# Performance work log

Measured on AMD Instinct MI355X. Metric: run time of the kernel, lower is better.

Reference implementation:

```python
import jax, jax.numpy as jnp
import numpy as np

BN_EPS = 1e-5


def _conv_bn_elu(x, w, b, bn_scale, bn_bias, bn_mean, bn_var):
    # 1x1 conv == channel-mixing matmul: x [B,C,H,W], w [O,C]
    y = jnp.einsum('bchw,oc->bohw', x, w) + b[None, :, None, None]
    inv = bn_scale * jax.lax.rsqrt(bn_var + BN_EPS)
    y = y * inv[None, :, None, None] + (bn_bias - bn_mean * inv)[None, :, None, None]
    return jax.nn.elu(y)


def setup_inputs() -> dict:
    key = jax.random.key(0)
    ks = jax.random.split(key, 24)
    B, C, H, W = 4, 128, 64, 64
    d = {}
    d['x_q'] = jax.random.normal(ks[0], (B, C, H, W), jnp.float32)
    d['x_k'] = jax.random.normal(ks[1], (B, C, H, W), jnp.float32)
    d['x_v'] = jax.random.normal(ks[2], (B, C, H, W), jnp.float32)
    scale = 1.0 / np.sqrt(C)
    i = 3
    for p in ('q', 'k', 'v'):
        d[f'{p}_w'] = jax.random.normal(ks[i], (C, C), jnp.float32) * scale; i += 1
        d[f'{p}_b'] = jax.random.normal(ks[i], (C,), jnp.float32) * 0.01; i += 1
        d[f'{p}_bn_scale'] = jnp.ones((C,), jnp.float32) + 0.1 * jax.random.normal(ks[i], (C,), jnp.float32); i += 1
        d[f'{p}_bn_bias'] = 0.1 * jax.random.normal(ks[i], (C,), jnp.float32); i += 1
        d[f'{p}_bn_mean'] = 0.1 * jax.random.normal(ks[i], (C,), jnp.float32); i += 1
        d[f'{p}_bn_var'] = jax.random.uniform(ks[i], (C,), jnp.float32, 0.5, 1.5); i += 1
    # torch inits gamma/beta to zero; use small nonzero values so output is informative
    d['gamma'] = jnp.array([0.5], jnp.float32)
    d['beta'] = jnp.array([0.5], jnp.float32)
    return d


def reference(x_q, x_k, x_v,
              q_w, q_b, q_bn_scale, q_bn_bias, q_bn_mean, q_bn_var,
              k_w, k_b, k_bn_scale, k_bn_bias, k_bn_mean, k_bn_var,
              v_w, v_b, v_bn_scale, v_bn_bias, v_bn_mean, v_bn_var,
              gamma, beta):
    B, C, Hv, Wv = x_v.shape
    q = _conv_bn_elu(x_q, q_w, q_b, q_bn_scale, q_bn_bias, q_bn_mean, q_bn_var).reshape(B, C, -1)  # [B,C,HWq]
    k = _conv_bn_elu(x_k, k_w, k_b, k_bn_scale, k_bn_bias, k_bn_mean, k_bn_var).reshape(B, C, -1)  # [B,C,HWk]
    v = _conv_bn_elu(x_v, v_w, v_b, v_bn_scale, v_bn_bias, v_bn_mean, v_bn_var).reshape(B, C, -1)  # [B,C,HWv]
    energy = jnp.einsum('bcq,bck->bqk', q, k)                 # [B,HWq,HWk] (no scaling, as in source)
    attention = jax.nn.softmax(energy, axis=-1)
    out = jnp.einsum('bck,bqk->bcq', v, attention)            # [B,C,HWq]
    out = out.reshape(B, C, Hv, Wv)
    return gamma * out + beta * x_v
```

## Files before the change

kernel.cpp:

```cpp
#include <hip/hip_runtime.h>

#define CC 128
#define SS 4096
#define L2E 1.44269504f

typedef _Float16 f16;
typedef f16 f16x8 __attribute__((ext_vector_type(8)));
typedef __fp16 h16x2 __attribute__((ext_vector_type(2)));
typedef float f32x4 __attribute__((ext_vector_type(4)));

struct PArg { const float *x, *w, *b, *sc, *bb, *bm, *bv; f16* out; };

__global__ __launch_bounds__(256) void projk(PArg A0, PArg A1, PArg A2) {
    const int p = blockIdx.y;
    PArg A = (p == 0) ? A0 : ((p == 1) ? A1 : A2);
    const int bx = blockIdx.x;
    const int b  = bx >> 6;
    const int s0 = (bx & 63) * 64;
    const int tid = threadIdx.x;
    const int w = tid >> 6, lane = tid & 63;
    const int n = lane & 15, g = lane >> 4;

    __shared__ f16 Xl[64][136];
    __shared__ f16 Wl[128][136];
    f16* Yl = &Wl[0][0];

#pragma unroll
    for (int i = 0; i < 8; ++i) {
        int vi = tid + i * 256;
        int c = vi >> 4, sq = (vi & 15) * 4;
        float4 v = *(const float4*)(A.x + ((size_t)b * CC + c) * SS + s0 + sq);
        Xl[sq + 0][c] = (f16)v.x; Xl[sq + 1][c] = (f16)v.y;
        Xl[sq + 2][c] = (f16)v.z; Xl[sq + 3][c] = (f16)v.w;
    }
#pragma unroll
    for (int i = 0; i < 8; ++i) {
        int vi = tid + i * 256;
        int o = vi >> 4, cq = (vi & 15) * 8;
        float iv = A.sc[o] * rsqrtf(A.bv[o] + 1e-5f);
        const float* wp = A.w + o * CC + cq;
        float4 a = *(const float4*)wp;
        float4 b4 = *(const float4*)(wp + 4);
        union { f16 h[8]; uint4 u; } pk;
        pk.h[0] = (f16)(a.x * iv);  pk.h[1] = (f16)(a.y * iv);
        pk.h[2] = (f16)(a.z * iv);  pk.h[3] = (f16)(a.w * iv);
        pk.h[4] = (f16)(b4.x * iv); pk.h[5] = (f16)(b4.y * iv);
        pk.h[6] = (f16)(b4.z * iv); pk.h[7] = (f16)(b4.w * iv);
        *(uint4*)&Wl[o][cq] = pk.u;
    }
    __syncthreads();

    if (p < 2) {
        const float qsc = (p == 0) ? L2E : 1.0f;
        f32x4 acc[2][4];
#pragma unroll
        for (int mt = 0; mt < 2; ++mt)
#pragma unroll
            for (int nt = 0; nt < 4; ++nt) acc[mt][nt] = (f32x4){0.f, 0.f, 0.f, 0.f};
#pragma unroll
        for (int ks = 0; ks < 4; ++ks) {
            f16x8 af[2], bf[4];
#pragma unroll
            for (int mt = 0; mt < 2; ++mt) af[mt] = *(const f16x8*)&Wl[w * 32 + mt * 16 + n][ks * 32 + g * 8];
#pragma unroll
            for (int nt = 0; nt < 4; ++nt) bf[nt] = *(const f16x8*)&Xl[nt * 16 + n][ks * 32 + g * 8];
#pragma unroll
            for (int mt = 0; mt < 2; ++mt)
#pragma unroll
                for (int nt = 0; nt < 4; ++nt)
                    acc[mt][nt] = __builtin_amdgcn_mfma_f32_16x16x32_f16(af[mt], bf[nt], acc[mt][nt], 0, 0, 0);
        }
        __syncthreads();
#pragma unroll
        for (int mt = 0; mt < 2; ++mt) {
            float ebr[4];
#pragma unroll
            for (int r = 0; r < 4; ++r) {
                int o = w * 32 + mt * 16 + g * 4 + r;
                float iv = A.sc[o] * rsqrtf(A.bv[o] + 1e-5f);
                ebr[r] = (A.b[o] - A.bm[o]) * iv + A.bb[o];
            }
#pragma unroll
            for (int nt = 0; nt < 4; ++nt) {
                union { f16 h[4]; uint2 u; } pk;
#pragma unroll
                for (int r = 0; r < 4; ++r) {
                    float y = acc[mt][nt][r] + ebr[r];
                    y = (y > 0.f) ? y : (__expf(y) - 1.f);
                    pk.h[r] = (f16)(y * qsc);
                }
                *(uint2*)&Yl[(nt * 16 + n) * 136 + w * 32 + mt * 16 + g * 4] = pk.u;
            }
        }
        __syncthreads();
#pragma unroll
        for (int i = 0; i < 4; ++i) {
            int vi = tid + i * 256;
            int s = vi >> 4, cl = (vi & 15) * 8;
            *(uint4*)&A.out[((size_t)b * SS + s0 + s) * CC + cl] = *(const uint4*)&Yl[s * 136 + cl];
        }
    } else {
        f32x4 acc[8];
#pragma unroll
        for (int nt = 0; nt < 8; ++nt) acc[nt] = (f32x4){0.f, 0.f, 0.f, 0.f};
#pragma unroll
        for (int ks = 0; ks < 4; ++ks) {
            f16x8 af = *(const f16x8*)&Xl[w * 16 + n][ks * 32 + g * 8];
#pragma unroll
            for (int nt = 0; nt < 8; ++nt) {
                f16x8 bf = *(const f16x8*)&Wl[nt * 16 + n][ks * 32 + g * 8];
                acc[nt] = __builtin_amdgcn_mfma_f32_16x16x32_f16(af, bf, acc[nt], 0, 0, 0);
            }
        }
        __syncthreads();
#pragma unroll
        for (int nt = 0; nt < 8; ++nt) {
            int o = nt * 16 + n;
            float iv = A.sc[o] * rsqrtf(A.bv[o] + 1e-5f);
            float ebc = (A.b[o] - A.bm[o]) * iv + A.bb[o];
            union { f16 h[4]; uint2 u; } pk;
#pragma unroll
            for (int r = 0; r < 4; ++r) {
                float y = acc[nt][r] + ebc;
                y = (y > 0.f) ? y : (__expf(y) - 1.f);
                pk.h[r] = (f16)y;
            }
            *(uint2*)&Yl[(nt * 16 + n) * 136 + w * 16 + g * 4] = pk.u;
        }
        __syncthreads();
#pragma unroll
        for (int i = 0; i < 4; ++i) {
            int vi = tid + i * 256;
            int o = vi >> 3, sl = (vi & 7) * 8;
            *(uint4*)&A.out[((size_t)b * CC + o) * SS + s0 + sl] = *(const uint4*)&Yl[o * 136 + sl];
        }
    }
}

__global__ __launch_bounds__(256, 3) void attnk(
    const f16* __restrict__ Qt, const f16* __restrict__ Kt, const f16* __restrict__ Vt,
    f16* __restrict__ Op, float* __restrict__ Ml)
{
    const int tid = threadIdx.x;
    const int bx = blockIdx.x;
    const int kh = bx & 7;
    const int b  = (bx >> 3) & 3;
    const int qt = bx >> 5;
    const int q0 = qt * 128;
    const int kbeg = kh * 512;

    __shared__ __align__(16) char arena[48128];
    const int w = tid >> 6, lane = tid & 63;
    const int n = lane & 15, g = lane >> 4;
    f16 (*Pw)[40] = (f16(*)[40])(arena + 37888 + w * 2560);

    f16x8 qf[2][4];
    {
        const f16* Qb = Qt + ((size_t)b * SS + q0 + w * 32) * CC;
#pragma unroll
        for (int qt2 = 0; qt2 < 2; ++qt2)
#pragma unroll
            for (int ks = 0; ks < 4; ++ks)
                qf[qt2][ks] = *(const f16x8*)&Qb[(qt2 * 16 + n) * CC + ks * 32 + g * 8];
    }

    f32x4 oacc[8][2];
#pragma unroll
    for (int mtc = 0; mtc < 8; ++mtc)
#pragma unroll
        for (int qt2 = 0; qt2 < 2; ++qt2) oacc[mtc][qt2] = (f32x4){0.f, 0.f, 0.f, 0.f};
    float mreg[2] = {-1e30f, -1e30f}, lsum[2] = {0.f, 0.f};

    const int rk0 = tid >> 4,        ck0 = (tid & 15) * 8;
    const int rk1 = (tid + 256) >> 4, ck1 = ((tid + 256) & 15) * 8;
    const int rv0 = tid >> 2,        cv0 = (tid & 3) * 8;
    const int rv1 = (tid + 256) >> 2, cv1 = ((tid + 256) & 3) * 8;

    {
        f16 (*Kl)[136] = (f16(*)[136])(arena);
        f16 (*Vl)[40]  = (f16(*)[40])(arena + 17408);
        *(uint4*)&Kl[rk0][ck0] = *(const uint4*)&Kt[((size_t)b * SS + kbeg + rk0) * CC + ck0];
        *(uint4*)&Kl[rk1][ck1] = *(const uint4*)&Kt[((size_t)b * SS + kbeg + rk1) * CC + ck1];
        *(uint4*)&Vl[rv0][cv0] = *(const uint4*)&Vt[((size_t)b * CC + rv0) * SS + kbeg + cv0];
        *(uint4*)&Vl[rv1][cv1] = *(const uint4*)&Vt[((size_t)b * CC + rv1) * SS + kbeg + cv1];
    }

    for (int kt = 0; kt < 16; ++kt) {
        const int cur = kt & 1;
        f16 (*Kl)[136] = (f16(*)[136])(arena + cur * 8704);
        f16 (*Vl)[40]  = (f16(*)[40])(arena + 17408 + cur * 10240);
        f16 (*Kn)[136] = (f16(*)[136])(arena + (1 - cur) * 8704);
        f16 (*Vn)[40]  = (f16(*)[40])(arena + 17408 + (1 - cur) * 10240);

        __syncthreads();

        uint4 nk0, nk1, nv0, nv1;
        if (kt < 15) {
            const int k1 = kbeg + (kt + 1) * 32;
            nk0 = *(const uint4*)&Kt[((size_t)b * SS + k1 + rk0) * CC + ck0];
            nk1 = *(const uint4*)&Kt[((size_t)b * SS + k1 + rk1) * CC + ck1];
            nv0 = *(const uint4*)&Vt[((size_t)b * CC + rv0) * SS + k1 + cv0];
            nv1 = *(const uint4*)&Vt[((size_t)b * CC + rv1) * SS + k1 + cv1];
        }

        f32x4 sacc[2][2];
#pragma unroll
        for (int kt2 = 0; kt2 < 2; ++kt2)
#pragma unroll
            for (int qt2 = 0; qt2 < 2; ++qt2) sacc[kt2][qt2] = (f32x4){0.f, 0.f, 0.f, 0.f};
#pragma unroll
        for (int ks = 0; ks < 4; ++ks) {
            f16x8 kf[2];
#pragma unroll
            for (int kt2 = 0; kt2 < 2; ++kt2) kf[kt2] = *(const f16x8*)&Kl[kt2 * 16 + n][ks * 32 + g * 8];
#pragma unroll
            for (int kt2 = 0; kt2 < 2; ++kt2)
#pragma unroll
                for (int qt2 = 0; qt2 < 2; ++qt2)
                    sacc[kt2][qt2] = __builtin_amdgcn_mfma_f32_16x16x32_f16(kf[kt2], qf[qt2][ks], sacc[kt2][qt2], 0, 0, 0);
        }

        if (kt < 15) {
            *(uint4*)&Kn[rk0][ck0] = nk0;
            *(uint4*)&Kn[rk1][ck1] = nk1;
            *(uint4*)&Vn[rv0][cv0] = nv0;
            *(uint4*)&Vn[rv1][cv1] = nv1;
        }

        float al[2];
#pragma unroll
        for (int qt2 = 0; qt2 < 2; ++qt2) {
            float v = sacc[0][qt2][0];
#pragma unroll
            for (int kt2 = 0; kt2 < 2; ++kt2)
#pragma unroll
                for (int r = 0; r < 4; ++r) v = fmaxf(v, sacc[kt2][qt2][r]);
            v = fmaxf(v, __shfl_xor(v, 16));
            v = fmaxf(v, __shfl_xor(v, 32));
            float mn = fmaxf(mreg[qt2], v);
            al[qt2] = exp2f(mreg[qt2] - mn);
            mreg[qt2] = mn;
            float rs = 0.f;
#pragma unroll
            for (int kt2 = 0; kt2 < 2; ++kt2) {
                float p0 = exp2f(sacc[kt2][qt2][0] - mn);
                float p1 = exp2f(sacc[kt2][qt2][1] - mn);
                float p2 = exp2f(sacc[kt2][qt2][2] - mn);
                float p3 = exp2f(sacc[kt2][qt2][3] - mn);
                rs += (p0 + p1) + (p2 + p3);
                union { h16x2 h[2]; uint2 u; } pk;
                pk.h[0] = __builtin_amdgcn_cvt_pkrtz(p0, p1);
                pk.h[1] = __builtin_amdgcn_cvt_pkrtz(p2, p3);
                *(uint2*)&Pw[qt2 * 16 + n][kt2 * 16 + g * 4] = pk.u;
            }
            lsum[qt2] = lsum[qt2] * al[qt2] + rs;
        }
#pragma unroll
        for (int mtc = 0; mtc < 8; ++mtc)
#pragma unroll
            for (int qt2 = 0; qt2 < 2; ++qt2)
#pragma unroll
                for (int r = 0; r < 4; ++r) oacc[mtc][qt2][r] *= al[qt2];

        {
            f16x8 pf[2];
#pragma unroll
            for (int qt2 = 0; qt2 < 2; ++qt2) pf[qt2] = *(const f16x8*)&Pw[qt2 * 16 + n][g * 8];
#pragma unroll
            for (int mtc = 0; mtc < 8; ++mtc) {
                f16x8 vf = *(const f16x8*)&Vl[mtc * 16 + n][g * 8];
#pragma unroll
                for (int qt2 = 0; qt2 < 2; ++qt2)
                    oacc[mtc][qt2] = __builtin_amdgcn_mfma_f32_16x16x32_f16(vf, pf[qt2], oacc[mtc][qt2], 0, 0, 0);
            }
        }
    }

    float lreg[2];
#pragma unroll
    for (int qt2 = 0; qt2 < 2; ++qt2) {
        float s = lsum[qt2];
        s += __shfl_xor(s, 16);
        s += __shfl_xor(s, 32);
        lreg[qt2] = s;
    }

    const int pidx = (b * 32 + qt) * 8 + kh;
    if (g == 0) {
        float* MlW = Ml + (size_t)pidx * 256;
#pragma unroll
        for (int qt2 = 0; qt2 < 2; ++qt2) {
            int q = w * 32 + qt2 * 16 + n;
            MlW[q]       = mreg[qt2];
            MlW[128 + q] = lreg[qt2];
        }
    }

    __syncthreads();
    f16 (*S2)[136] = (f16(*)[136])arena;
#pragma unroll
    for (int mtc = 0; mtc < 8; ++mtc)
#pragma unroll
        for (int qt2 = 0; qt2 < 2; ++qt2)
#pragma unroll
            for (int r = 0; r < 4; ++r)
                S2[mtc * 16 + g * 4 + r][w * 32 + qt2 * 16 + n] = (f16)oacc[mtc][qt2][r];
    __syncthreads();
    f16* OpW = Op + (size_t)pidx * 16384;
#pragma unroll
    for (int i = 0; i < 8; ++i) {
        int vi = tid + i * 256;
        int c = vi >> 4, qq = (vi & 15) * 8;
        *(uint4*)&OpW[c * 128 + qq] = *(const uint4*)&S2[c][qq];
    }
}

__global__ __launch_bounds__(256) void mrgk(
    const f16* __restrict__ Op, const float* __restrict__ Ml,
    const float* __restrict__ xv, const float* __restrict__ gp, const float* __restrict__ bp,
    float* __restrict__ out)
{
    const int bx = blockIdx.x;
    const int cg = bx & 3, bqt = bx >> 2;
    const int b = bqt >> 5, qt = bqt & 31;
    const int tid = threadIdx.x;

    __shared__ float winv[8][128];

    if (tid < 128) {
        const int q = tid;
        const float* ml = Ml + (size_t)bqt * 8 * 256;
        float m = -1e30f;
#pragma unroll
        for (int k2 = 0; k2 < 8; ++k2) m = fmaxf(m, ml[k2 * 256 + q]);
        float wt[8], tot = 0.f;
#pragma unroll
        for (int k2 = 0; k2 < 8; ++k2) {
            wt[k2] = exp2f(ml[k2 * 256 + q] - m);
            tot += wt[k2] * ml[k2 * 256 + 128 + q];
        }
        float inv = 1.f / tot;
#pragma unroll
        for (int k2 = 0; k2 < 8; ++k2) winv[k2][q] = wt[k2] * inv;
    }
    __syncthreads();

    const float gm = gp[0], bb = bp[0];
    const int cl = tid >> 4, qg = tid & 15;
    const f16* O = Op + (size_t)bqt * 8 * 16384;

#pragma unroll
    for (int cp = 0; cp < 2; ++cp) {
        const int c = cg * 32 + cp * 16 + cl;
        float acc[8];
#pragma unroll
        for (int j = 0; j < 8; ++j) acc[j] = 0.f;
#pragma unroll
        for (int k2 = 0; k2 < 8; ++k2) {
            union { uint4 u; f16 h[8]; } ov;
            ov.u = *(const uint4*)&O[k2 * 16384 + c * 128 + qg * 8];
            float4 wa = *(const float4*)&winv[k2][qg * 8];
            float4 wb = *(const float4*)&winv[k2][qg * 8 + 4];
            acc[0] += wa.x * (float)ov.h[0];
            acc[1] += wa.y * (float)ov.h[1];
            acc[2] += wa.z * (float)ov.h[2];
            acc[3] += wa.w * (float)ov.h[3];
            acc[4] += wb.x * (float)ov.h[4];
            acc[5] += wb.y * (float)ov.h[5];
            acc[6] += wb.z * (float)ov.h[6];
            acc[7] += wb.w * (float)ov.h[7];
        }
        size_t idx = ((size_t)(b * CC + c)) * SS + qt * 128 + qg * 8;
        float4 xa = *(const float4*)&xv[idx];
        float4 xb = *(const float4*)&xv[idx + 4];
        float4 oa = { gm * acc[0] + bb * xa.x, gm * acc[1] + bb * xa.y,
                      gm * acc[2] + bb * xa.z, gm * acc[3] + bb * xa.w };
        float4 ob = { gm * acc[4] + bb * xb.x, gm * acc[5] + bb * xb.y,
                      gm * acc[6] + bb * xb.z, gm * acc[7] + bb * xb.w };
        *(float4*)&out[idx]     = oa;
        *(float4*)&out[idx + 4] = ob;
    }
}

extern "C" void kernel_launch(void* const* d_in, const int* in_sizes, int n_in,
                              void* d_out, int out_size, void* d_ws, size_t ws_size,
                              hipStream_t stream) {
    (void)in_sizes; (void)n_in; (void)out_size; (void)ws_size;

    const size_t TEN = (size_t)4 * SS * CC;
    f16* Qt = (f16*)d_ws;
    f16* Kt = Qt + TEN;
    f16* Vt = Kt + TEN;
    f16* Op = Vt + TEN;
    float* Ml = (float*)(Op + (size_t)1024 * 16384);

    PArg aq = { (const float*)d_in[0], (const float*)d_in[3],  (const float*)d_in[4],
                (const float*)d_in[5], (const float*)d_in[6],  (const float*)d_in[7],
                (const float*)d_in[8],  Qt };
    PArg ak = { (const float*)d_in[1], (const float*)d_in[9],  (const float*)d_in[10],
                (const float*)d_in[11], (const float*)d_in[12], (const float*)d_in[13],
                (const float*)d_in[14], Kt };
    PArg av = { (const float*)d_in[2], (const float*)d_in[15], (const float*)d_in[16],
                (const float*)d_in[17], (const float*)d_in[18], (const float*)d_in[19],
                (const float*)d_in[20], Vt };

    hipLaunchKernelGGL(projk, dim3(256, 3), dim3(256), 0, stream, aq, ak, av);
    hipLaunchKernelGGL(attnk, dim3(1024), dim3(256), 0, stream, Qt, Kt, Vt, Op, Ml);
    hipLaunchKernelGGL(mrgk, dim3(512), dim3(256), 0, stream,
                       Op, Ml, (const float*)d_in[2], (const float*)d_in[21],
                       (const float*)d_in[22], (float*)d_out);
}
```

Baseline: 182.4 us.

## Use direct global-to-LDS loads with XOR-swizzled K/V/P tiles in attention

Replaces the register-staged K/V prefetch (global load into registers, later store to LDS) with global_load_lds 16-byte direct-to-LDS loads. Padded LDS rows are replaced by XOR-swizzled unpadded layouts for K, V and the P scratch tile, which shrinks the LDS arena. The aim is to cut register pressure and VGPR-to-LDS store instructions and to avoid bank conflicts, possibly allowing more overlap. It relies on the direct-LDS load write pattern (per-wave contiguous placement) matching the swizzle, and the synchronization must still order those async writes before their reads.

```diff
diff --git a/kernel.cpp b/kernel.cpp
--- a/kernel.cpp
+++ b/kernel.cpp
@@ -8,6 +8,12 @@
 typedef f16 f16x8 __attribute__((ext_vector_type(8)));
 typedef __fp16 h16x2 __attribute__((ext_vector_type(2)));
 typedef float f32x4 __attribute__((ext_vector_type(4)));
+
+__device__ __forceinline__ void gld16(const void* g, void* l) {
+    __builtin_amdgcn_global_load_lds(
+        (const __attribute__((address_space(1))) void*)(uintptr_t)g,
+        (__attribute__((address_space(3))) void*)(uint32_t)(uintptr_t)l, 16, 0, 0);
+}
 
 struct PArg { const float *x, *w, *b, *sc, *bb, *bm, *bv; f16* out; };
 
@@ -149,10 +155,10 @@
     const int q0 = qt * 128;
     const int kbeg = kh * 512;
 
-    __shared__ __align__(16) char arena[48128];
+    __shared__ __align__(16) char arena[40960];
     const int w = tid >> 6, lane = tid & 63;
     const int n = lane & 15, g = lane >> 4;
-    f16 (*Pw)[40] = (f16(*)[40])(arena + 37888 + w * 2560);
+    char* Pb = arena + 32768 + (w << 11);
 
     f16x8 qf[2][4];
     {
@@ -171,36 +177,39 @@
         for (int qt2 = 0; qt2 < 2; ++qt2) oacc[mtc][qt2] = (f32x4){0.f, 0.f, 0.f, 0.f};
     float mreg[2] = {-1e30f, -1e30f}, lsum[2] = {0.f, 0.f};
 
-    const int rk0 = tid >> 4,        ck0 = (tid & 15) * 8;
-    const int rk1 = (tid + 256) >> 4, ck1 = ((tid + 256) & 15) * 8;
-    const int rv0 = tid >> 2,        cv0 = (tid & 3) * 8;
-    const int rv1 = (tid + 256) >> 2, cv1 = ((tid + 256) & 3) * 8;
+    const int rk0 = tid >> 4;
+    const int cgK = ((tid & 15) ^ (rk0 & 7)) * 8;
+    const int rv0 = tid >> 2;
+    const int cgV = ((tid & 3) ^ (rv0 & 3)) * 8;
 
     {
-        f16 (*Kl)[136] = (f16(*)[136])(arena);
-        f16 (*Vl)[40]  = (f16(*)[40])(arena + 17408);
-        *(uint4*)&Kl[rk0][ck0] = *(const uint4*)&Kt[((size_t)b * SS + kbeg + rk0) * CC + ck0];
-        *(uint4*)&Kl[rk1][ck1] = *(const uint4*)&Kt[((size_t)b * SS + kbeg + rk1) * CC + ck1];
-        *(uint4*)&Vl[rv0][cv0] = *(const uint4*)&Vt[((size_t)b * CC + rv0) * SS + kbeg + cv0];
-        *(uint4*)&Vl[rv1][cv1] = *(const uint4*)&Vt[((size_t)b * CC + rv1) * SS + kbeg + cv1];
+        char* kd = arena + (w << 10);
+        char* vd = arena + 16384 + (w << 10);
+        const f16* gK = &Kt[((size_t)b * SS + kbeg + rk0) * CC + cgK];
+        const f16* gV = &Vt[((size_t)b * CC + rv0) * SS + kbeg + cgV];
+        gld16(gK, kd);
+        gld16(gK + (size_t)16 * CC, kd + 4096);
+        gld16(gV, vd);
+        gld16(gV + (size_t)64 * SS, vd + 4096);
     }
 
     for (int kt = 0; kt < 16; ++kt) {
         const int cur = kt & 1;
-        f16 (*Kl)[136] = (f16(*)[136])(arena + cur * 8704);
-        f16 (*Vl)[40]  = (f16(*)[40])(arena + 17408 + cur * 10240);
-        f16 (*Kn)[136] = (f16(*)[136])(arena + (1 - cur) * 8704);
-        f16 (*Vn)[40]  = (f16(*)[40])(arena + 17408 + (1 - cur) * 10240);
+        char* Kb = arena + cur * 8192;
+        char* Vb = arena + 16384 + cur * 8192;
 
         __syncthreads();
 
-        uint4 nk0, nk1, nv0, nv1;
         if (kt < 15) {
             const int k1 = kbeg + (kt + 1) * 32;
-            nk0 = *(const uint4*)&Kt[((size_t)b * SS + k1 + rk0) * CC + ck0];
-            nk1 = *(const uint4*)&Kt[((size_t)b * SS + k1 + rk1) * CC + ck1];
-            nv0 = *(const uint4*)&Vt[((size_t)b * CC + rv0) * SS + k1 + cv0];
-            nv1 = *(const uint4*)&Vt[((size_t)b * CC + rv1) * SS + k1 + cv1];
+            char* kd = arena + (1 - cur) * 8192 + (w << 10);
+            char* vd = arena + 16384 + (1 - cur) * 8192 + (w << 10);
+            const f16* gK = &Kt[((size_t)b * SS + k1 + rk0) * CC + cgK];
+            const f16* gV = &Vt[((size_t)b * CC + rv0) * SS + k1 + cgV];
+            gld16(gK, kd);
+            gld16(gK + (size_t)16 * CC, kd + 4096);
+            gld16(gV, vd);
+            gld16(gV + (size_t)64 * SS, vd + 4096);
         }
 
         f32x4 sacc[2][2];
@@ -212,19 +221,13 @@
         for (int ks = 0; ks < 4; ++ks) {
             f16x8 kf[2];
 #pragma unroll
-            for (int kt2 = 0; kt2 < 2; ++kt2) kf[kt2] = *(const f16x8*)&Kl[kt2 * 16 + n][ks * 32 + g * 8];
+            for (int kt2 = 0; kt2 < 2; ++kt2)
+                kf[kt2] = *(const f16x8*)(Kb + (kt2 * 16 + n) * 256 + (((ks * 4 + g) ^ (n & 7)) << 4));
 #pragma unroll
             for (int kt2 = 0; kt2 < 2; ++kt2)
 #pragma unroll
                 for (int qt2 = 0; qt2 < 2; ++qt2)
                     sacc[kt2][qt2] = __builtin_amdgcn_mfma_f32_16x16x32_f16(kf[kt2], qf[qt2][ks], sacc[kt2][qt2], 0, 0, 0);
-        }
-
-        if (kt < 15) {
-            *(uint4*)&Kn[rk0][ck0] = nk0;
-            *(uint4*)&Kn[rk1][ck1] = nk1;
-            *(uint4*)&Vn[rv0][cv0] = nv0;
-            *(uint4*)&Vn[rv1][cv1] = nv1;
         }
 
         float al[2];
@@ -251,7 +254,9 @@
                 union { h16x2 h[2]; uint2 u; } pk;
                 pk.h[0] = __builtin_amdgcn_cvt_pkrtz(p0, p1);
                 pk.h[1] = __builtin_amdgcn_cvt_pkrtz(p2, p3);
-                *(uint2*)&Pw[qt2 * 16 + n][kt2 * 16 + g * 4] = pk.u;
+                *(uint2*)(Pb + (qt2 * 16 + n) * 64
+                             + (((kt2 * 2 + (g >> 1)) ^ (n & 3)) << 4)
+                             + ((g & 1) << 3)) = pk.u;
             }
             lsum[qt2] = lsum[qt2] * al[qt2] + rs;
         }
@@ -263,12 +268,14 @@
                 for (int r = 0; r < 4; ++r) oacc[mtc][qt2][r] *= al[qt2];
 
         {
+            const int gx = ((g ^ (n & 3)) << 4);
             f16x8 pf[2];
 #pragma unroll
-            for (int qt2 = 0; qt2 < 2; ++qt2) pf[qt2] = *(const f16x8*)&Pw[qt2 * 16 + n][g * 8];
+            for (int qt2 = 0; qt2 < 2; ++qt2)
+                pf[qt2] = *(const f16x8*)(Pb + (qt2 * 16 + n) * 64 + gx);
 #pragma unroll
             for (int mtc = 0; mtc < 8; ++mtc) {
-                f16x8 vf = *(const f16x8*)&Vl[mtc * 16 + n][g * 8];
+                f16x8 vf = *(const f16x8*)(Vb + (mtc * 16 + n) * 64 + gx);
 #pragma unroll
                 for (int qt2 = 0; qt2 < 2; ++qt2)
                     oacc[mtc][qt2] = __builtin_amdgcn_mfma_f32_16x16x32_f16(vf, pf[qt2], oacc[mtc][qt2], 0, 0, 0);
```

Result: no change. 184.9 us (+1.3%).
